# Kernel optimization log

Hardware: AMD Instinct MI355X
Metric: run time of the kernel (lower is better)

The kernel has to match this reference:

```python
import jax, jax.numpy as jnp
import numpy as np

T, B, N, D = 32, 8, 256, 512
TAU = 2.0   # LIF membrane time constant
VTH = 1.0   # spike threshold
ALPHA = 4.0 # surrogate-gradient sharpness


def setup_inputs() -> dict:
    key = jax.random.key(0)
    k0, k1, k2 = jax.random.split(key, 3)
    scale = 1.0 / np.sqrt(D)
    return {
        "x": jax.random.normal(k0, (T, B, N, D), jnp.float32),
        "tr_mx": jnp.zeros((B, N, D), jnp.float32),            # initial membrane state
        "W_lif": jax.random.normal(k1, (D, D), jnp.float32) * scale,
        "b_lif": jnp.zeros((D,), jnp.float32),
        "W_rec": jax.random.normal(k2, (D, D), jnp.float32) * scale,  # recon2 weight (d_ff=D -> patch_size=D)
        "b_rec": jnp.zeros((D,), jnp.float32),
    }


def _spike(v):
    # Heaviside forward, sigmoid surrogate backward (standard SNN straight-through)
    s = jax.nn.sigmoid(ALPHA * v)
    return s + jax.lax.stop_gradient((v > 0).astype(v.dtype) - s)


def reference(x, tr_mx, W_lif, b_lif, W_rec, b_rec):
    # MemoryUpdate.replay: tau-decayed LIF recurrence over time, emitting spike gate per step
    inp = jnp.einsum('tbnd,de->tbne', x, W_lif) + b_lif   # [T,B,N,D] input current

    def step(mem, i_t):
        mem = mem + (i_t - mem) / TAU        # leaky integration
        sp = _spike(mem - VTH)               # fire
        mem = mem * (1.0 - sp)               # hard reset
        return mem, sp

    _, sp_seq = jax.lax.scan(step, tr_mx, inp)  # sp_seq: [T,B,N,D]

    g = x * (1.0 - sp_seq)                       # gated residual
    rec_x = jnp.einsum('tbnd,dp->tbnp', g, W_rec) + b_rec  # recon2 on flattened (T*B, N, D)
    return rec_x
```

## Files before the change

### kernel.cpp

```cpp
#include <hip/hip_runtime.h>
#include <hip/hip_bf16.h>


#define TT 32
#define CH 8
#define BB 8
#define NN 256
#define DD 512

typedef __attribute__((ext_vector_type(8))) short short8;
typedef __attribute__((ext_vector_type(4))) float f32x4;

__device__ __forceinline__ unsigned short f2bf(float f) {
    __hip_bfloat16 h = __float2bfloat16(f);
    return *reinterpret_cast<unsigned short*>(&h);
}

__global__ void cast_transpose_wr(const float* __restrict__ Wr,
                                  unsigned short* __restrict__ Wt) {
    int idx = blockIdx.x * 256 + threadIdx.x;
    int d = idx >> 9;
    int p = idx & 511;
    Wt[p * DD + d] = f2bf(Wr[idx]);
}

template<bool UW>
__global__ __launch_bounds__(256, 2) void lif_decoder_v10(
    const float* __restrict__ x,
    const float* __restrict__ tr_mx,
    const float* __restrict__ Wl,
    const float* __restrict__ bl,
    const float* __restrict__ Wr,
    const float* __restrict__ br,
    const unsigned short* __restrict__ Wt,
    float* __restrict__ out)
{
    __shared__ __align__(16) float xs[2 * CH * DD];
    __shared__ __align__(16) unsigned msk[2 * DD];

    const int tid = threadIdx.x;
    const int tg  = tid >> 7;
    const int tl  = tid & 127;
    const int e0  = tl * 4;
    const int tok = blockIdx.x * 2 + tg;
    const size_t base = (size_t)tok * DD;
    const size_t st   = (size_t)BB * NN * DD;

    {
        float acc[CH][4];
        float4 m4 = *reinterpret_cast<const float4*>(&tr_mx[base + e0]);
        float m[4] = {m4.x, m4.y, m4.z, m4.w};
        unsigned mc[4] = {0u, 0u, 0u, 0u};

        const float4 blv = *reinterpret_cast<const float4*>(&bl[e0]);
        const float blr[4] = {blv.x, blv.y, blv.z, blv.w};

        #pragma unroll 1
        for (int tgc = 0; tgc < 4; ++tgc) {
            #pragma unroll
            for (int r = 0; r < 8; ++r) {
                const int flat = r * 256 + tid;
                const int q    = flat >> 10;
                const int rem  = flat & 1023;
                const int trow = rem >> 7;
                const int c4   = rem & 127;
                const float4 v = *reinterpret_cast<const float4*>(
                    &x[(size_t)(tgc * CH + trow) * st
                       + (size_t)(blockIdx.x * 2 + q) * DD + c4 * 4]);
                *reinterpret_cast<float4*>(&xs[(q * CH + trow) * DD + c4 * 4]) = v;
            }
            __syncthreads();

            #pragma unroll
            for (int i = 0; i < CH; ++i)
                #pragma unroll
                for (int e = 0; e < 4; ++e) acc[i][e] = blr[e];

            const float* xsl = &xs[tg * CH * DD];

            #pragma unroll 2
            for (int d = 0; d < DD; d += 4) {
                const float4 w0 = *reinterpret_cast<const float4*>(&Wl[(size_t)(d + 0) * DD + e0]);
                const float4 w1 = *reinterpret_cast<const float4*>(&Wl[(size_t)(d + 1) * DD + e0]);
                const float4 w2 = *reinterpret_cast<const float4*>(&Wl[(size_t)(d + 2) * DD + e0]);
                const float4 w3 = *reinterpret_cast<const float4*>(&Wl[(size_t)(d + 3) * DD + e0]);
                #pragma unroll
                for (int i = 0; i < CH; ++i) {
                    const float4 xv = *reinterpret_cast<const float4*>(&xsl[i * DD + d]);
                    acc[i][0] = fmaf(xv.x, w0.x, acc[i][0]);
                    acc[i][1] = fmaf(xv.x, w0.y, acc[i][1]);
                    acc[i][2] = fmaf(xv.x, w0.z, acc[i][2]);
                    acc[i][3] = fmaf(xv.x, w0.w, acc[i][3]);
                    acc[i][0] = fmaf(xv.y, w1.x, acc[i][0]);
                    acc[i][1] = fmaf(xv.y, w1.y, acc[i][1]);
                    acc[i][2] = fmaf(xv.y, w1.z, acc[i][2]);
                    acc[i][3] = fmaf(xv.y, w1.w, acc[i][3]);
                    acc[i][0] = fmaf(xv.z, w2.x, acc[i][0]);
                    acc[i][1] = fmaf(xv.z, w2.y, acc[i][1]);
                    acc[i][2] = fmaf(xv.z, w2.z, acc[i][2]);
                    acc[i][3] = fmaf(xv.z, w2.w, acc[i][3]);
                    acc[i][0] = fmaf(xv.w, w3.x, acc[i][0]);
                    acc[i][1] = fmaf(xv.w, w3.y, acc[i][1]);
                    acc[i][2] = fmaf(xv.w, w3.z, acc[i][2]);
                    acc[i][3] = fmaf(xv.w, w3.w, acc[i][3]);
                }
            }
            __syncthreads();

            #pragma unroll
            for (int i = 0; i < CH; ++i) {
                const int t = tgc * CH + i;
                #pragma unroll
                for (int e = 0; e < 4; ++e) {
                    m[e] = m[e] + (acc[i][e] - m[e]) * 0.5f;
                    const float s = (m[e] - 1.0f > 0.0f) ? 1.0f : 0.0f;
                    mc[e] |= (s > 0.0f) ? (1u << t) : 0u;
                    m[e] *= (1.0f - s);
                }
            }
        }

        #pragma unroll
        for (int e = 0; e < 4; ++e) msk[tg * DD + e0 + e] = mc[e];
    }
    __syncthreads();

    {
        const int wv   = tid >> 6;
        const int lane = tid & 63;
        const int qB   = wv >> 1;
        const int hB   = wv & 1;
        const int lcol = lane & 15;
        const int lkg  = lane >> 4;
        const int tA   = hB * 16 + lcol;
        const size_t baseB = (size_t)(blockIdx.x * 2 + qB) * DD;
        const unsigned* mq = &msk[qB * DD];
        const float* xrow = &x[(size_t)tA * st + baseB];

        #pragma unroll 1
        for (int pass = 0; pass < 4; ++pass) {
            const int colb = pass * 128;
            f32x4 acc[8];
            #pragma unroll
            for (int nt = 0; nt < 8; ++nt) {
                const float b = br[colb + nt * 16 + lcol];
                acc[nt] = (f32x4){b, b, b, b};
            }

            #pragma unroll
            for (int ks = 0; ks < 16; ++ks) {
                const int kb = ks * 32 + lkg * 8;
                const float4 x0 = *reinterpret_cast<const float4*>(&xrow[kb]);
                const float4 x1 = *reinterpret_cast<const float4*>(&xrow[kb + 4]);
                const uint4 m0 = *reinterpret_cast<const uint4*>(&mq[kb]);
                const uint4 m1 = *reinterpret_cast<const uint4*>(&mq[kb + 4]);
                short8 a;
                a[0] = (short)f2bf(((m0.x >> tA) & 1u) ? 0.0f : x0.x);
                a[1] = (short)f2bf(((m0.y >> tA) & 1u) ? 0.0f : x0.y);
                a[2] = (short)f2bf(((m0.z >> tA) & 1u) ? 0.0f : x0.z);
                a[3] = (short)f2bf(((m0.w >> tA) & 1u) ? 0.0f : x0.w);
                a[4] = (short)f2bf(((m1.x >> tA) & 1u) ? 0.0f : x1.x);
                a[5] = (short)f2bf(((m1.y >> tA) & 1u) ? 0.0f : x1.y);
                a[6] = (short)f2bf(((m1.z >> tA) & 1u) ? 0.0f : x1.z);
                a[7] = (short)f2bf(((m1.w >> tA) & 1u) ? 0.0f : x1.w);

                #pragma unroll
                for (int nt = 0; nt < 8; ++nt) {
                    const int col = colb + nt * 16 + lcol;
                    short8 bf;
                    if (UW) {
                        bf = *reinterpret_cast<const short8*>(&Wt[(size_t)col * DD + kb]);
                    } else {
                        #pragma unroll
                        for (int j = 0; j < 8; ++j)
                            bf[j] = (short)f2bf(Wr[(size_t)(kb + j) * DD + col]);
                    }
                    acc[nt] = __builtin_amdgcn_mfma_f32_16x16x32_bf16(a, bf, acc[nt], 0, 0, 0);
                }
            }

            #pragma unroll
            for (int nt = 0; nt < 8; ++nt) {
                const int col = colb + nt * 16 + lcol;
                #pragma unroll
                for (int r = 0; r < 4; ++r) {
                    const int t = hB * 16 + lkg * 4 + r;
                    out[(size_t)t * st + baseB + col] = acc[nt][r];
                }
            }
        }
    }
}

extern "C" void kernel_launch(void* const* d_in, const int* in_sizes, int n_in,
                              void* d_out, int out_size, void* d_ws, size_t ws_size,
                              hipStream_t stream) {
    const float* x     = (const float*)d_in[0];
    const float* tr_mx = (const float*)d_in[1];
    const float* Wl    = (const float*)d_in[2];
    const float* bl    = (const float*)d_in[3];
    const float* Wr    = (const float*)d_in[4];
    const float* br    = (const float*)d_in[5];
    float* out = (float*)d_out;

    const size_t wt_bytes = (size_t)DD * DD * 2;
    dim3 grid(BB * NN / 2);
    dim3 block(256);

    if (ws_size >= wt_bytes) {
        unsigned short* Wt = (unsigned short*)d_ws;
        cast_transpose_wr<<<dim3(1024), dim3(256), 0, stream>>>(Wr, Wt);
        lif_decoder_v10<true><<<grid, block, 0, stream>>>(x, tr_mx, Wl, bl, Wr, br, Wt, out);
    } else {
        lif_decoder_v10<false><<<grid, block, 0, stream>>>(x, tr_mx, Wl, bl, Wr, br, nullptr, out);
    }
}
```

Measured before the change: 782.2 us.

## Split fused LIF kernel into separate spike-mask and MFMA decoder kernels

```diff
diff --git a/kernel.cpp b/kernel.cpp
--- a/kernel.cpp
+++ b/kernel.cpp
@@ -24,16 +24,206 @@
     Wt[p * DD + d] = f2bf(Wr[idx]);
 }
 
-template<bool UW>
-__global__ __launch_bounds__(256, 2) void lif_decoder_v10(
+__global__ __launch_bounds__(128, 4) void lif_phaseA(
     const float* __restrict__ x,
     const float* __restrict__ tr_mx,
     const float* __restrict__ Wl,
     const float* __restrict__ bl,
+    unsigned* __restrict__ gmsk)
+{
+    __shared__ __align__(16) float xs[CH * 256];
+
+    const int tid = threadIdx.x;
+    const int tok = blockIdx.x;
+    const int e0  = tid * 4;
+    const size_t base = (size_t)tok * DD;
+    const size_t st   = (size_t)BB * NN * DD;
+
+    float acc[CH][4];
+    float4 m4 = *reinterpret_cast<const float4*>(&tr_mx[base + e0]);
+    float m[4] = {m4.x, m4.y, m4.z, m4.w};
+    unsigned mc[4] = {0u, 0u, 0u, 0u};
+
+    const float4 blv = *reinterpret_cast<const float4*>(&bl[e0]);
+    const float blr[4] = {blv.x, blv.y, blv.z, blv.w};
+
+    #pragma unroll 1
+    for (int tg = 0; tg < 4; ++tg) {
+        #pragma unroll
+        for (int i = 0; i < CH; ++i)
+            #pragma unroll
+            for (int e = 0; e < 4; ++e) acc[i][e] = blr[e];
+
+        #pragma unroll 1
+        for (int h = 0; h < 2; ++h) {
+            #pragma unroll
+            for (int r = 0; r < 4; ++r) {
+                const int flat = r * 128 + tid;
+                const int row  = flat >> 6;
+                const int c4   = flat & 63;
+                const float4 v = *reinterpret_cast<const float4*>(
+                    &x[(size_t)(tg * CH + row) * st + base + h * 256 + c4 * 4]);
+                *reinterpret_cast<float4*>(&xs[row * 256 + c4 * 4]) = v;
+            }
+            __syncthreads();
+
+            #pragma unroll 2
+            for (int dd_ = 0; dd_ < 256; dd_ += 4) {
+                const int d = h * 256 + dd_;
+                const float4 w0 = *reinterpret_cast<const float4*>(&Wl[(size_t)(d + 0) * DD + e0]);
+                const float4 w1 = *reinterpret_cast<const float4*>(&Wl[(size_t)(d + 1) * DD + e0]);
+                const float4 w2 = *reinterpret_cast<const float4*>(&Wl[(size_t)(d + 2) * DD + e0]);
+                const float4 w3 = *reinterpret_cast<const float4*>(&Wl[(size_t)(d + 3) * DD + e0]);
+                #pragma unroll
+                for (int i = 0; i < CH; ++i) {
+                    const float4 xv = *reinterpret_cast<const float4*>(&xs[i * 256 + dd_]);
+                    acc[i][0] = fmaf(xv.x, w0.x, acc[i][0]);
+                    acc[i][1] = fmaf(xv.x, w0.y, acc[i][1]);
+                    acc[i][2] = fmaf(xv.x, w0.z, acc[i][2]);
+                    acc[i][3] = fmaf(xv.x, w0.w, acc[i][3]);
+                    acc[i][0] = fmaf(xv.y, w1.x, acc[i][0]);
+                    acc[i][1] = fmaf(xv.y, w1.y, acc[i][1]);
+                    acc[i][2] = fmaf(xv.y, w1.z, acc[i][2]);
+                    acc[i][3] = fmaf(xv.y, w1.w, acc[i][3]);
+                    acc[i][0] = fmaf(xv.z, w2.x, acc[i][0]);
+                    acc[i][1] = fmaf(xv.z, w2.y, acc[i][1]);
+                    acc[i][2] = fmaf(xv.z, w2.z, acc[i][2]);
+                    acc[i][3] = fmaf(xv.z, w2.w, acc[i][3]);
+                    acc[i][0] = fmaf(xv.w, w3.x, acc[i][0]);
+                    acc[i][1] = fmaf(xv.w, w3.y, acc[i][1]);
+                    acc[i][2] = fmaf(xv.w, w3.z, acc[i][2]);
+                    acc[i][3] = fmaf(xv.w, w3.w, acc[i][3]);
+                }
+            }
+            __syncthreads();
+        }
+
+        #pragma unroll
+        for (int i = 0; i < CH; ++i) {
+            const int t = tg * CH + i;
+            #pragma unroll
+            for (int e = 0; e < 4; ++e) {
+                m[e] = m[e] + (acc[i][e] - m[e]) * 0.5f;
+                const float s = (m[e] - 1.0f > 0.0f) ? 1.0f : 0.0f;
+                mc[e] |= (s > 0.0f) ? (1u << t) : 0u;
+                m[e] *= (1.0f - s);
+            }
+        }
+    }
+
+    uint4 mv;
+    mv.x = mc[0]; mv.y = mc[1]; mv.z = mc[2]; mv.w = mc[3];
+    *reinterpret_cast<uint4*>(&gmsk[base + e0]) = mv;
+}
+
+#define CP 132
+
+template<bool UW>
+__global__ __launch_bounds__(256, 2) void lif_phaseB(
+    const float* __restrict__ x,
     const float* __restrict__ Wr,
     const float* __restrict__ br,
     const unsigned short* __restrict__ Wt,
+    const unsigned* __restrict__ gmsk,
     float* __restrict__ out)
+{
+    __shared__ __align__(16) unsigned ms[2 * DD];
+    __shared__ __align__(16) float cs[2 * TT * CP];
+
+    const int tid = threadIdx.x;
+    const size_t st = (size_t)BB * NN * DD;
+
+    {
+        const uint4 v = *reinterpret_cast<const uint4*>(
+            &gmsk[(size_t)blockIdx.x * 2 * DD + tid * 4]);
+        *reinterpret_cast<uint4*>(&ms[tid * 4]) = v;
+    }
+    __syncthreads();
+
+    const int wv   = tid >> 6;
+    const int lane = tid & 63;
+    const int qB   = wv >> 1;
+    const int hB   = wv & 1;
+    const int lcol = lane & 15;
+    const int lkg  = lane >> 4;
+    const int tA   = hB * 16 + lcol;
+    const size_t baseB = (size_t)(blockIdx.x * 2 + qB) * DD;
+    const unsigned* mq = &ms[qB * DD];
+    const float* xrow = &x[(size_t)tA * st + baseB];
+
+    #pragma unroll 1
+    for (int pass = 0; pass < 4; ++pass) {
+        const int colb = pass * 128;
+        f32x4 acc[8];
+        #pragma unroll
+        for (int nt = 0; nt < 8; ++nt) {
+            const float b = br[colb + nt * 16 + lcol];
+            acc[nt] = (f32x4){b, b, b, b};
+        }
+
+        #pragma unroll
+        for (int ks = 0; ks < 16; ++ks) {
+            const int kb = ks * 32 + lkg * 8;
+            const float4 x0 = *reinterpret_cast<const float4*>(&xrow[kb]);
+            const float4 x1 = *reinterpret_cast<const float4*>(&xrow[kb + 4]);
+            const uint4 m0 = *reinterpret_cast<const uint4*>(&mq[kb]);
+            const uint4 m1 = *reinterpret_cast<const uint4*>(&mq[kb + 4]);
+            short8 a;
+            a[0] = (short)f2bf(((m0.x >> tA) & 1u) ? 0.0f : x0.x);
+            a[1] = (short)f2bf(((m0.y >> tA) & 1u) ? 0.0f : x0.y);
+            a[2] = (short)f2bf(((m0.z >> tA) & 1u) ? 0.0f : x0.z);
+            a[3] = (short)f2bf(((m0.w >> tA) & 1u) ? 0.0f : x0.w);
+            a[4] = (short)f2bf(((m1.x >> tA) & 1u) ? 0.0f : x1.x);
+            a[5] = (short)f2bf(((m1.y >> tA) & 1u) ? 0.0f : x1.y);
+            a[6] = (short)f2bf(((m1.z >> tA) & 1u) ? 0.0f : x1.z);
+            a[7] = (short)f2bf(((m1.w >> tA) & 1u) ? 0.0f : x1.w);
+
+            #pragma unroll
+            for (int nt = 0; nt < 8; ++nt) {
+                const int col = colb + nt * 16 + lcol;
+                short8 bf;
+                if (UW) {
+                    bf = *reinterpret_cast<const short8*>(&Wt[(size_t)col * DD + kb]);
+                } else {
+                    #pragma unroll
+                    for (int j = 0; j < 8; ++j)
+                        bf[j] = (short)f2bf(Wr[(size_t)(kb + j) * DD + col]);
+                }
+                acc[nt] = __builtin_amdgcn_mfma_f32_16x16x32_bf16(a, bf, acc[nt], 0, 0, 0);
+            }
+        }
+
+        #pragma unroll
+        for (int nt = 0; nt < 8; ++nt) {
+            #pragma unroll
+            for (int r = 0; r < 4; ++r) {
+                const int t = hB * 16 + lkg * 4 + r;
+                cs[(qB * TT + t) * CP + nt * 16 + lcol] = acc[nt][r];
+            }
+        }
+        __syncthreads();
+
+        #pragma unroll
+        for (int k = 0; k < 8; ++k) {
+            const int flat = k * 256 + tid;
+            const int seg  = flat >> 5;
+            const int wi   = flat & 31;
+            const int q    = seg >> 5;
+            const int t    = seg & 31;
+            float4 v = *reinterpret_cast<const float4*>(&cs[(q * TT + t) * CP + wi * 4]);
+            *reinterpret_cast<float4*>(
+                &out[(size_t)t * st + (size_t)(blockIdx.x * 2 + q) * DD + colb + wi * 4]) = v;
+        }
+        __syncthreads();
+    }
+}
+
+template<bool UW>
+__global__ __launch_bounds__(256, 2) void lif_decoder_v10(
+    const float* __restrict__ x, const float* __restrict__ tr_mx,
+    const float* __restrict__ Wl, const float* __restrict__ bl,
+    const float* __restrict__ Wr, const float* __restrict__ br,
+    const unsigned short* __restrict__ Wt, float* __restrict__ out)
 {
     __shared__ __align__(16) float xs[2 * CH * DD];
     __shared__ __align__(16) unsigned msk[2 * DD];
@@ -51,7 +241,6 @@
         float4 m4 = *reinterpret_cast<const float4*>(&tr_mx[base + e0]);
         float m[4] = {m4.x, m4.y, m4.z, m4.w};
         unsigned mc[4] = {0u, 0u, 0u, 0u};
-
         const float4 blv = *reinterpret_cast<const float4*>(&bl[e0]);
         const float blr[4] = {blv.x, blv.y, blv.z, blv.w};
 
@@ -77,7 +266,6 @@
                 for (int e = 0; e < 4; ++e) acc[i][e] = blr[e];
 
             const float* xsl = &xs[tg * CH * DD];
-
             #pragma unroll 2
             for (int d = 0; d < DD; d += 4) {
                 const float4 w0 = *reinterpret_cast<const float4*>(&Wl[(size_t)(d + 0) * DD + e0]);
@@ -119,7 +307,6 @@
                 }
             }
         }
-
         #pragma unroll
         for (int e = 0; e < 4; ++e) msk[tg * DD + e0 + e] = mc[e];
     }
@@ -146,7 +333,6 @@
                 const float b = br[colb + nt * 16 + lcol];
                 acc[nt] = (f32x4){b, b, b, b};
             }
-
             #pragma unroll
             for (int ks = 0; ks < 16; ++ks) {
                 const int kb = ks * 32 + lkg * 8;
@@ -163,7 +349,6 @@
                 a[5] = (short)f2bf(((m1.y >> tA) & 1u) ? 0.0f : x1.y);
                 a[6] = (short)f2bf(((m1.z >> tA) & 1u) ? 0.0f : x1.z);
                 a[7] = (short)f2bf(((m1.w >> tA) & 1u) ? 0.0f : x1.w);
-
                 #pragma unroll
                 for (int nt = 0; nt < 8; ++nt) {
                     const int col = colb + nt * 16 + lcol;
@@ -178,7 +363,6 @@
                     acc[nt] = __builtin_amdgcn_mfma_f32_16x16x32_bf16(a, bf, acc[nt], 0, 0, 0);
                 }
             }
-
             #pragma unroll
             for (int nt = 0; nt < 8; ++nt) {
                 const int col = colb + nt * 16 + lcol;
@@ -203,15 +387,20 @@
     const float* br    = (const float*)d_in[5];
     float* out = (float*)d_out;
 
-    const size_t wt_bytes = (size_t)DD * DD * 2;
-    dim3 grid(BB * NN / 2);
-    dim3 block(256);
-
-    if (ws_size >= wt_bytes) {
+    const size_t msk_bytes = (size_t)BB * NN * DD * 4;
+    const size_t wt_bytes  = (size_t)DD * DD * 2;
+
+    if (ws_size >= msk_bytes + wt_bytes) {
+        unsigned* gmsk = (unsigned*)d_ws;
+        unsigned short* Wt = (unsigned short*)((char*)d_ws + msk_bytes);
+        cast_transpose_wr<<<dim3(1024), dim3(256), 0, stream>>>(Wr, Wt);
+        lif_phaseA<<<dim3(BB * NN), dim3(128), 0, stream>>>(x, tr_mx, Wl, bl, gmsk);
+        lif_phaseB<true><<<dim3(BB * NN / 2), dim3(256), 0, stream>>>(x, Wr, br, Wt, gmsk, out);
+    } else if (ws_size >= wt_bytes) {
         unsigned short* Wt = (unsigned short*)d_ws;
         cast_transpose_wr<<<dim3(1024), dim3(256), 0, stream>>>(Wr, Wt);
-        lif_decoder_v10<true><<<grid, block, 0, stream>>>(x, tr_mx, Wl, bl, Wr, br, Wt, out);
+        lif_decoder_v10<true><<<dim3(BB * NN / 2), dim3(256), 0, stream>>>(x, tr_mx, Wl, bl, Wr, br, Wt, out);
     } else {
-        lif_decoder_v10<false><<<grid, block, 0, stream>>>(x, tr_mx, Wl, bl, Wr, br, nullptr, out);
-    }
-}
+        lif_decoder_v10<false><<<dim3(BB * NN / 2), dim3(256), 0, stream>>>(x, tr_mx, Wl, bl, Wr, br, nullptr, out);
+    }
+}
```

After: 884.8 us. 1.13x slower.
